# Optimization experiments

Measured on AMD Instinct MI355X. Metric: run time of the kernel, lower is better.

The kernel has to match this reference:

```python
import jax, jax.numpy as jnp
import numpy as np

BLOCK_SIZE = 64
SPARSITY_RATIO = 0.5


def _band_mask(seq_len, block_size, sparsity_ratio):
    # Block (i, j) is computed iff max(0, i-w) <= j < min(nb, i+w), w = int(nb*ratio).
    nb = seq_len // block_size
    w = int(nb * sparsity_ratio)
    ib = jnp.arange(nb)
    bm = (ib[None, :] >= ib[:, None] - w) & (ib[None, :] < ib[:, None] + w)  # [nb, nb]
    return jnp.repeat(jnp.repeat(bm, block_size, axis=0), block_size, axis=1)  # [S, S]


def setup_inputs() -> dict:
    key = jax.random.key(0)
    kq, kk, kv = jax.random.split(key, 3)
    B, S, D = 4, 4096, 128
    return {
        "query": jax.random.normal(kq, (B, S, D), dtype=jnp.float32),
        "key": jax.random.normal(kk, (B, S, D), dtype=jnp.float32),
        "value": jax.random.normal(kv, (B, S, D), dtype=jnp.float32),
    }


def reference(query, key, value):
    B, S, D = query.shape
    mask = _band_mask(S, BLOCK_SIZE, SPARSITY_RATIO)  # [S, S] bool
    scores = jnp.einsum('bqd,bkd->bqk', query, key)  # [B, S, S]
    # Outside-band entries stay exactly 0 (NOT -inf) — matches torch.zeros init.
    scores = jnp.where(mask[None, :, :], scores, jnp.zeros((), scores.dtype))
    probs = jax.nn.softmax(scores, axis=-1)
    return jnp.matmul(probs, value)  # [B, S, D]
```

## Files before the change

kernel.cpp:

```cpp
#include <hip/hip_runtime.h>


typedef _Float16 f16;
typedef __attribute__((ext_vector_type(8))) _Float16 f16x8;
typedef __attribute__((ext_vector_type(4))) _Float16 f16x4;
typedef __attribute__((ext_vector_type(4))) float f32x4;

#define MFMA16(a, b, c) __builtin_amdgcn_mfma_f32_16x16x32_f16((a), (b), (c), 0, 0, 0)

#define BATCH 4
#define SEQ   4096
#define DIM   128
#define NB    64
#define WBAND 32
#define LOG2E 1.44269504088896f
#define DTHR  8.0f
#define TSTR  72

#define TILE  16384
#define CHUNKS 8
#define PART_STRIDE 16896

__device__ __forceinline__ void gl16(const char* g, char* l) {
  __builtin_amdgcn_global_load_lds(
      (const __attribute__((address_space(1))) void*)g,
      (__attribute__((address_space(3))) void*)l, 16, 0, 0);
}

__global__ __launch_bounds__(256) void convert_kernel(
    const float* __restrict__ K, const float* __restrict__ V,
    f16* __restrict__ KF, f16* __restrict__ VF, float* __restrict__ BS) {
  __shared__ f16 T[128 * TSTR];
  const int blk = blockIdx.x;
  const int b = blk >> 6, jb = blk & 63;
  const int s0 = jb * 64;
  const int t = threadIdx.x;

#pragma unroll
  for (int i = 0; i < 8; ++i) {
    int idx = t + i * 256;
    int row = idx >> 5;
    int c4 = (idx & 31) * 4;
    float4 v = *(const float4*)(V + (size_t)(b * SEQ + s0 + row) * DIM + c4);
    T[(c4 + 0) * TSTR + row] = (f16)v.x;
    T[(c4 + 1) * TSTR + row] = (f16)v.y;
    T[(c4 + 2) * TSTR + row] = (f16)v.z;
    T[(c4 + 3) * TSTR + row] = (f16)v.w;
  }

  char* kt = (char*)KF + (size_t)blk * TILE;
#pragma unroll
  for (int i = 0; i < 4; ++i) {
    int idx = t + i * 256;
    int frag = idx >> 6, lane = idx & 63;
    int ks = frag >> 2, jt = frag & 3;
    int row = jt * 16 + (lane & 15);
    int d0 = ks * 32 + (lane >> 4) * 8;
    const float* src = K + ((size_t)(b * SEQ + s0 + row)) * DIM + d0;
    float4 a = *(const float4*)src;
    float4 d = *(const float4*)(src + 4);
    f16x8 h = {(f16)a.x, (f16)a.y, (f16)a.z, (f16)a.w,
               (f16)d.x, (f16)d.y, (f16)d.z, (f16)d.w};
    *(f16x8*)(kt + idx * 16) = h;
  }
  __syncthreads();

  char* vt = (char*)VF + (size_t)blk * TILE;
#pragma unroll
  for (int i = 0; i < 4; ++i) {
    int idx = t + i * 256;
    int frag = idx >> 6, lane = idx & 63;
    int ks2 = frag >> 3, nt = frag & 7;
    int d = nt * 16 + (lane & 15);
    int k0 = ks2 * 32 + ((lane >> 4) & 3) * 4;
    f16x4 x = *(const f16x4*)(T + d * TSTR + k0);
    f16x4 y = *(const f16x4*)(T + d * TSTR + k0 + 16);
    f16x8 h = {x[0], x[1], x[2], x[3], y[0], y[1], y[2], y[3]};
    *(f16x8*)(vt + idx * 16) = h;
  }

  if (t < 128) {
    float s = 0.f;
    for (int k = 0; k < 64; ++k) s += (float)T[t * TSTR + k];
    BS[(b * NB + jb) * DIM + t] = s;
  }
}

__global__ __launch_bounds__(256, 2) void attn_kernel(
    const float* __restrict__ Q, const f16* __restrict__ KF,
    const f16* __restrict__ VF, char* __restrict__ PART) {
  __shared__ __align__(16) char smem[16384];

  const int id = blockIdx.x;
  const int lin = (id & 7) * 128 + (id >> 3);
  const int ck = lin & 7;
  const int pair = lin >> 3;
  const int b = pair >> 5, p = pair & 31;

  const int t = threadIdx.x;
  const int w = t >> 6, l = t & 63, lg = l >> 4, ll = l & 15;
  const int half = w >> 1, qh = w & 1;
  const int myib = p * 2 + half;

  const int jloU = max(0, p * 2 - WBAND);
  const int jhiU = min(NB, p * 2 + 1 + WBAND);
  const int lenU = jhiU - jloU;
  const int base = lenU >> 3, rem = lenU & 7;
  const int j0 = jloU + ck * base + min(ck, rem);
  const int nloc = base + (ck < rem ? 1 : 0);
  const int mylo = max(0, myib - WBAND);
  const int myhi = min(NB, myib + WBAND);

  f16x8 qf[2][4];
#pragma unroll
  for (int s = 0; s < 2; ++s) {
    const float* qrow =
        Q + ((size_t)(b * SEQ + myib * 64 + qh * 32 + s * 16 + ll)) * DIM;
#pragma unroll
    for (int ks = 0; ks < 4; ++ks) {
      int d0 = ks * 32 + lg * 8;
      float4 a = *(const float4*)(qrow + d0);
      float4 cc = *(const float4*)(qrow + d0 + 4);
      float vv[8] = {a.x, a.y, a.z, a.w, cc.x, cc.y, cc.z, cc.w};
#pragma unroll
      for (int e = 0; e < 8; ++e) qf[s][ks][e] = (f16)(vv[e] * LOG2E);
    }
  }

  float m2[2] = {0.f, 0.f};
  float ell[2] = {0.f, 0.f};
  f32x4 o[2][8];
#pragma unroll
  for (int s = 0; s < 2; ++s)
#pragma unroll
    for (int nt = 0; nt < 8; ++nt) o[s][nt] = (f32x4){0.f, 0.f, 0.f, 0.f};

  auto stageK = [&](int jb) {
    const char* kg = (const char*)KF + ((size_t)(b * NB + jb)) * TILE + t * 16;
#pragma unroll
    for (int i = 0; i < 4; ++i) gl16(kg + i * 4096, smem + t * 16 + i * 4096);
  };

  stageK(j0);
  __syncthreads();

  for (int tt = 0; tt < nloc; ++tt) {
    const int j = j0 + tt;
    if (j >= mylo && j < myhi) {
      const char* vt =
          (const char*)VF + ((size_t)(b * NB + j)) * TILE + (size_t)l * 16;
      f16x8 vr0[8], vr1[8];
#pragma unroll
      for (int nt = 0; nt < 8; ++nt)
        vr0[nt] = *(const f16x8*)(vt + nt * 1024);
#pragma unroll
      for (int nt = 0; nt < 8; ++nt)
        vr1[nt] = *(const f16x8*)(vt + (8 + nt) * 1024);

      f32x4 sacc[2][4];
#pragma unroll
      for (int s = 0; s < 2; ++s)
#pragma unroll
        for (int jt = 0; jt < 4; ++jt) sacc[s][jt] = (f32x4){0.f, 0.f, 0.f, 0.f};

      __builtin_amdgcn_s_setprio(1);
#pragma unroll
      for (int ks = 0; ks < 4; ++ks) {
#pragma unroll
        for (int jt = 0; jt < 4; ++jt) {
          f16x8 kf = *(const f16x8*)(smem + (ks * 4 + jt) * 1024 + l * 16);
          sacc[0][jt] = MFMA16(kf, qf[0][ks], sacc[0][jt]);
          sacc[1][jt] = MFMA16(kf, qf[1][ks], sacc[1][jt]);
        }
      }
      __builtin_amdgcn_s_setprio(0);

      f16x8 pa[2][2];
#pragma unroll
      for (int s = 0; s < 2; ++s) {
        float vm = fmaxf(fmaxf(sacc[s][0][0], sacc[s][0][1]),
                         fmaxf(sacc[s][0][2], sacc[s][0][3]));
#pragma unroll
        for (int jt = 1; jt < 4; ++jt)
#pragma unroll
          for (int r = 0; r < 4; ++r) vm = fmaxf(vm, sacc[s][jt][r]);
        vm = fmaxf(vm, __shfl_xor(vm, 16));
        vm = fmaxf(vm, __shfl_xor(vm, 32));

        if (__any(vm - m2[s] > DTHR)) {
          float nm = fmaxf(m2[s], vm);
          float scl = __builtin_amdgcn_exp2f(m2[s] - nm);
          m2[s] = nm;
          ell[s] *= scl;
          float sb[4];
#pragma unroll
          for (int r = 0; r < 4; ++r) sb[r] = __shfl(scl, lg * 4 + r);
#pragma unroll
          for (int nt = 0; nt < 8; ++nt)
#pragma unroll
            for (int r = 0; r < 4; ++r) o[s][nt][r] *= sb[r];
        }

        float rsum = 0.f;
#pragma unroll
        for (int ks2 = 0; ks2 < 2; ++ks2) {
          f16x8 pv;
#pragma unroll
          for (int u = 0; u < 2; ++u)
#pragma unroll
            for (int r = 0; r < 4; ++r) {
              float pe = __builtin_amdgcn_exp2f(sacc[s][ks2 * 2 + u][r] - m2[s]);
              rsum += pe;
              pv[u * 4 + r] = (f16)pe;
            }
          pa[s][ks2] = pv;
        }
        ell[s] += rsum;
      }

      __builtin_amdgcn_s_setprio(1);
#pragma unroll
      for (int nt = 0; nt < 8; ++nt) {
        o[0][nt] = MFMA16(pa[0][0], vr0[nt], o[0][nt]);
        o[1][nt] = MFMA16(pa[1][0], vr0[nt], o[1][nt]);
      }
#pragma unroll
      for (int nt = 0; nt < 8; ++nt) {
        o[0][nt] = MFMA16(pa[0][1], vr1[nt], o[0][nt]);
        o[1][nt] = MFMA16(pa[1][1], vr1[nt], o[1][nt]);
      }
      __builtin_amdgcn_s_setprio(0);
    }

    __syncthreads();
    if (tt + 1 < nloc) stageK(j0 + tt + 1);
    __syncthreads();
  }

#pragma unroll
  for (int s = 0; s < 2; ++s) {
    ell[s] += __shfl_xor(ell[s], 16);
    ell[s] += __shfl_xor(ell[s], 32);
  }

  char* pb = PART + ((size_t)((pair * CHUNKS + ck) * 2 + half)) * PART_STRIDE;
#pragma unroll
  for (int s = 0; s < 2; ++s)
#pragma unroll
    for (int g = 0; g < 4; ++g) {
      f16x8 hh;
#pragma unroll
      for (int r = 0; r < 4; ++r) {
        hh[r] = (f16)o[s][2 * g][r];
        hh[4 + r] = (f16)o[s][2 * g + 1][r];
      }
      *(f16x8*)(pb + qh * 8192 + ((s * 4 + g) * 64 + l) * 16) = hh;
    }
  if (lg == 0) {
#pragma unroll
    for (int s = 0; s < 2; ++s)
      *(float2*)(pb + 16384 + (qh * 32 + s * 16 + ll) * 8) =
          make_float2(m2[s], ell[s]);
  }
}

__global__ __launch_bounds__(256) void merge_kernel(
    const char* __restrict__ PART, const float* __restrict__ BS,
    float* __restrict__ Out) {
  __shared__ float VoutS[DIM];
  __shared__ float mlS[CHUNKS][64][2];

  const int id = blockIdx.x;
  const int lin = (id & 7) * 32 + (id >> 3);
  const int pair = lin >> 1, half = lin & 1;
  const int b = pair >> 5;
  const int ib = (pair & 31) * 2 + half;
  const int t = threadIdx.x;
  const int l = t & 63, lg = (t >> 4) & 3, ll = t & 15;
  const int sub = (t >> 6) & 1, qh = t >> 7;

  const int jlo = max(0, ib - WBAND);
  const int jhi = min(NB, ib + WBAND);
  const float cnt_out = (float)(SEQ - (jhi - jlo) * 64);

  if (t < DIM) {
    float s = 0.f;
    for (int j = 0; j < jlo; ++j) s += BS[(b * NB + j) * DIM + t];
    for (int j = jhi; j < NB; ++j) s += BS[(b * NB + j) * DIM + t];
    VoutS[t] = s;
  }

  const size_t pb0 = ((size_t)(pair * CHUNKS * 2 + half)) * PART_STRIDE;
  for (int i = t; i < CHUNKS * 64; i += 256) {
    int k = i >> 6, row = i & 63;
    *(float2*)&mlS[k][row][0] = *(const float2*)(
        PART + pb0 + (size_t)k * 2 * PART_STRIDE + 16384 + row * 8);
  }
  __syncthreads();

  float aw[4][CHUNKS], en[4], inv[4];
#pragma unroll
  for (int r = 0; r < 4; ++r) {
    int row = qh * 32 + sub * 16 + lg * 4 + r;
    float M = mlS[0][row][0];
#pragma unroll
    for (int k = 1; k < CHUNKS; ++k) M = fmaxf(M, mlS[k][row][0]);
    en[r] = __builtin_amdgcn_exp2f(-M);
    float den = cnt_out * en[r];
#pragma unroll
    for (int k = 0; k < CHUNKS; ++k) {
      aw[r][k] = __builtin_amdgcn_exp2f(mlS[k][row][0] - M);
      den += aw[r][k] * mlS[k][row][1];
    }
    inv[r] = 1.f / den;
  }

  float acc[8][4];
#pragma unroll
  for (int nt = 0; nt < 8; ++nt)
#pragma unroll
    for (int r = 0; r < 4; ++r) acc[nt][r] = 0.f;

  for (int k = 0; k < CHUNKS; ++k) {
    const char* oc = PART + pb0 + (size_t)k * 2 * PART_STRIDE + qh * 8192;
#pragma unroll
    for (int g = 0; g < 4; ++g) {
      f16x8 h = *(const f16x8*)(oc + ((sub * 4 + g) * 64 + l) * 16);
#pragma unroll
      for (int r = 0; r < 4; ++r) {
        acc[2 * g][r] += aw[r][k] * (float)h[r];
        acc[2 * g + 1][r] += aw[r][k] * (float)h[4 + r];
      }
    }
  }

  const int q0 = ib * 64;
#pragma unroll
  for (int nt = 0; nt < 8; ++nt) {
    int col = nt * 16 + ll;
    float vout = VoutS[col];
#pragma unroll
    for (int r = 0; r < 4; ++r) {
      int row = qh * 32 + sub * 16 + lg * 4 + r;
      Out[((size_t)(b * SEQ + q0 + row)) * DIM + col] =
          (acc[nt][r] + en[r] * vout) * inv[r];
    }
  }
}

extern "C" void kernel_launch(void* const* d_in, const int* in_sizes, int n_in,
                              void* d_out, int out_size, void* d_ws, size_t ws_size,
                              hipStream_t stream) {
  const float* Q = (const float*)d_in[0];
  const float* K = (const float*)d_in[1];
  const float* V = (const float*)d_in[2];
  float* Out = (float*)d_out;

  char* ws = (char*)d_ws;
  f16* KF = (f16*)ws;
  f16* VF = (f16*)(ws + (size_t)BATCH * NB * TILE);
  float* BS = (float*)(ws + 2 * (size_t)BATCH * NB * TILE);
  char* PART = ws + 2 * (size_t)BATCH * NB * TILE + (size_t)BATCH * NB * DIM * 4;

  convert_kernel<<<dim3(BATCH * NB), 256, 0, stream>>>(K, V, KF, VF, BS);
  attn_kernel<<<dim3(BATCH * NB / 2 * CHUNKS), 256, 0, stream>>>(Q, KF, VF, PART);
  merge_kernel<<<dim3(BATCH * NB), 256, 0, stream>>>(PART, BS, Out);
}
```

Measured before the change: 66.83 us.

## Split attention into producer/consumer warps with LDS-staged probabilities

Each block now handles one query block instead of a pair. Two waves compute QK^T and the softmax and write f16 probabilities plus rescale factors into double-buffered LDS. The other two waves consume the previous tile's probabilities and do the PV MFMAs, each over half of the head dimension. This pipelines the two GEMM phases across waves, removes the pair-union wasted iterations, and raises the occupancy target to 3. The cost is more LDS, a one-tile lag, unconditional rescaling of the output every tile, and a changed V fragment layout in the convert kernel.

```diff
diff --git a/kernel.cpp b/kernel.cpp
--- a/kernel.cpp
+++ b/kernel.cpp
@@ -14,12 +14,16 @@
 #define NB    64
 #define WBAND 32
 #define LOG2E 1.44269504088896f
-#define DTHR  8.0f
 #define TSTR  72
+#define PSTR  72
 
 #define TILE  16384
 #define CHUNKS 8
 #define PART_STRIDE 16896
+
+#define POFF  16384
+#define PSZ   9216
+#define SOFF  34816
 
 __device__ __forceinline__ void gl16(const char* g, char* l) {
   __builtin_amdgcn_global_load_lds(
@@ -72,10 +76,8 @@
     int frag = idx >> 6, lane = idx & 63;
     int ks2 = frag >> 3, nt = frag & 7;
     int d = nt * 16 + (lane & 15);
-    int k0 = ks2 * 32 + ((lane >> 4) & 3) * 4;
-    f16x4 x = *(const f16x4*)(T + d * TSTR + k0);
-    f16x4 y = *(const f16x4*)(T + d * TSTR + k0 + 16);
-    f16x8 h = {x[0], x[1], x[2], x[3], y[0], y[1], y[2], y[3]};
+    int k0 = ks2 * 32 + (lane >> 4) * 8;
+    f16x8 h = *(const f16x8*)(T + d * TSTR + k0);
     *(f16x8*)(vt + idx * 16) = h;
   }
 
@@ -86,83 +88,113 @@
   }
 }
 
-__global__ __launch_bounds__(256, 2) void attn_kernel(
+__global__ __launch_bounds__(256, 3) void attn_kernel(
     const float* __restrict__ Q, const f16* __restrict__ KF,
     const f16* __restrict__ VF, char* __restrict__ PART) {
-  __shared__ __align__(16) char smem[16384];
+  __shared__ __align__(16) char smem[35328];
 
   const int id = blockIdx.x;
-  const int lin = (id & 7) * 128 + (id >> 3);
+  const int lin = (id & 7) * 256 + (id >> 3);
   const int ck = lin & 7;
-  const int pair = lin >> 3;
-  const int b = pair >> 5, p = pair & 31;
+  const int blk = lin >> 3;
+  const int b = blk >> 6, ib = blk & 63;
 
   const int t = threadIdx.x;
   const int w = t >> 6, l = t & 63, lg = l >> 4, ll = l & 15;
-  const int half = w >> 1, qh = w & 1;
-  const int myib = p * 2 + half;
-
-  const int jloU = max(0, p * 2 - WBAND);
-  const int jhiU = min(NB, p * 2 + 1 + WBAND);
-  const int lenU = jhiU - jloU;
-  const int base = lenU >> 3, rem = lenU & 7;
-  const int j0 = jloU + ck * base + min(ck, rem);
+  const int wr = (w + (id & 3)) & 3;
+  const bool isP = (wr < 2);
+  const int qh = wr & 1;
+  const int dh = wr & 1;
+
+  const int jlo = max(0, ib - WBAND);
+  const int jhi = min(NB, ib + WBAND);
+  const int n = jhi - jlo;
+  const int base = n >> 3, rem = n & 7;
+  const int j0 = jlo + ck * base + min(ck, rem);
   const int nloc = base + (ck < rem ? 1 : 0);
-  const int mylo = max(0, myib - WBAND);
-  const int myhi = min(NB, myib + WBAND);
+
+  f16* P0 = (f16*)(smem + POFF);
+  f16* P1 = (f16*)(smem + POFF + PSZ);
+  float* S0 = (float*)(smem + SOFF);
+  float* S1 = (float*)(smem + SOFF + 256);
 
   f16x8 qf[2][4];
-#pragma unroll
-  for (int s = 0; s < 2; ++s) {
-    const float* qrow =
-        Q + ((size_t)(b * SEQ + myib * 64 + qh * 32 + s * 16 + ll)) * DIM;
-#pragma unroll
-    for (int ks = 0; ks < 4; ++ks) {
-      int d0 = ks * 32 + lg * 8;
-      float4 a = *(const float4*)(qrow + d0);
-      float4 cc = *(const float4*)(qrow + d0 + 4);
-      float vv[8] = {a.x, a.y, a.z, a.w, cc.x, cc.y, cc.z, cc.w};
-#pragma unroll
-      for (int e = 0; e < 8; ++e) qf[s][ks][e] = (f16)(vv[e] * LOG2E);
-    }
-  }
-
   float m2[2] = {0.f, 0.f};
   float ell[2] = {0.f, 0.f};
-  f32x4 o[2][8];
-#pragma unroll
-  for (int s = 0; s < 2; ++s)
-#pragma unroll
-    for (int nt = 0; nt < 8; ++nt) o[s][nt] = (f32x4){0.f, 0.f, 0.f, 0.f};
-
-  auto stageK = [&](int jb) {
+  if (isP) {
+#pragma unroll
+    for (int s = 0; s < 2; ++s) {
+      const float* qrow =
+          Q + ((size_t)(b * SEQ + ib * 64 + qh * 32 + s * 16 + ll)) * DIM;
+#pragma unroll
+      for (int ks = 0; ks < 4; ++ks) {
+        int d0 = ks * 32 + lg * 8;
+        float4 a = *(const float4*)(qrow + d0);
+        float4 cc = *(const float4*)(qrow + d0 + 4);
+        float vv[8] = {a.x, a.y, a.z, a.w, cc.x, cc.y, cc.z, cc.w};
+#pragma unroll
+        for (int e = 0; e < 8; ++e) qf[s][ks][e] = (f16)(vv[e] * LOG2E);
+      }
+    }
+  }
+
+  f32x4 o[4][4];
+#pragma unroll
+  for (int qt2 = 0; qt2 < 4; ++qt2)
+#pragma unroll
+    for (int ntl = 0; ntl < 4; ++ntl) o[qt2][ntl] = (f32x4){0.f, 0.f, 0.f, 0.f};
+
+  auto stage = [&](int jb) {
     const char* kg = (const char*)KF + ((size_t)(b * NB + jb)) * TILE + t * 16;
 #pragma unroll
     for (int i = 0; i < 4; ++i) gl16(kg + i * 4096, smem + t * 16 + i * 4096);
   };
 
-  stageK(j0);
+  auto consume = [&](int tj) {
+    const f16* Pb = (tj & 1) ? P1 : P0;
+    const float* Sb = (tj & 1) ? S1 : S0;
+    const char* vt = (const char*)VF + ((size_t)(b * NB + j0 + tj)) * TILE +
+                     (size_t)l * 16;
+    f16x8 vbf[2][4];
+#pragma unroll
+    for (int ks2 = 0; ks2 < 2; ++ks2)
+#pragma unroll
+      for (int ntl = 0; ntl < 4; ++ntl)
+        vbf[ks2][ntl] = *(const f16x8*)(vt + (ks2 * 8 + dh * 4 + ntl) * 1024);
+#pragma unroll
+    for (int qt2 = 0; qt2 < 4; ++qt2) {
+      f32x4 sv = *(const f32x4*)(Sb + qt2 * 16 + lg * 4);
+#pragma unroll
+      for (int ntl = 0; ntl < 4; ++ntl)
+#pragma unroll
+        for (int r = 0; r < 4; ++r) o[qt2][ntl][r] *= sv[r];
+    }
+    __builtin_amdgcn_s_setprio(1);
+#pragma unroll
+    for (int qt2 = 0; qt2 < 4; ++qt2) {
+#pragma unroll
+      for (int ks2 = 0; ks2 < 2; ++ks2) {
+        f16x8 paf = *(const f16x8*)((const char*)Pb +
+                                    (qt2 * 16 + ll) * (PSTR * 2) +
+                                    (ks2 * 32 + lg * 8) * 2);
+#pragma unroll
+        for (int ntl = 0; ntl < 4; ++ntl)
+          o[qt2][ntl] = MFMA16(paf, vbf[ks2][ntl], o[qt2][ntl]);
+      }
+    }
+    __builtin_amdgcn_s_setprio(0);
+  };
+
+  stage(j0);
   __syncthreads();
 
   for (int tt = 0; tt < nloc; ++tt) {
-    const int j = j0 + tt;
-    if (j >= mylo && j < myhi) {
-      const char* vt =
-          (const char*)VF + ((size_t)(b * NB + j)) * TILE + (size_t)l * 16;
-      f16x8 vr0[8], vr1[8];
-#pragma unroll
-      for (int nt = 0; nt < 8; ++nt)
-        vr0[nt] = *(const f16x8*)(vt + nt * 1024);
-#pragma unroll
-      for (int nt = 0; nt < 8; ++nt)
-        vr1[nt] = *(const f16x8*)(vt + (8 + nt) * 1024);
-
+    if (isP) {
       f32x4 sacc[2][4];
 #pragma unroll
       for (int s = 0; s < 2; ++s)
 #pragma unroll
         for (int jt = 0; jt < 4; ++jt) sacc[s][jt] = (f32x4){0.f, 0.f, 0.f, 0.f};
-
       __builtin_amdgcn_s_setprio(1);
 #pragma unroll
       for (int ks = 0; ks < 4; ++ks) {
@@ -175,7 +207,8 @@
       }
       __builtin_amdgcn_s_setprio(0);
 
-      f16x8 pa[2][2];
+      f16* Pb = (tt & 1) ? P1 : P0;
+      float* Sb = (tt & 1) ? S1 : S0;
 #pragma unroll
       for (int s = 0; s < 2; ++s) {
         float vm = fmaxf(fmaxf(sacc[s][0][0], sacc[s][0][1]),
@@ -186,81 +219,66 @@
           for (int r = 0; r < 4; ++r) vm = fmaxf(vm, sacc[s][jt][r]);
         vm = fmaxf(vm, __shfl_xor(vm, 16));
         vm = fmaxf(vm, __shfl_xor(vm, 32));
-
-        if (__any(vm - m2[s] > DTHR)) {
-          float nm = fmaxf(m2[s], vm);
-          float scl = __builtin_amdgcn_exp2f(m2[s] - nm);
-          m2[s] = nm;
-          ell[s] *= scl;
-          float sb[4];
-#pragma unroll
-          for (int r = 0; r < 4; ++r) sb[r] = __shfl(scl, lg * 4 + r);
-#pragma unroll
-          for (int nt = 0; nt < 8; ++nt)
-#pragma unroll
-            for (int r = 0; r < 4; ++r) o[s][nt][r] *= sb[r];
+        float nm = fmaxf(m2[s], vm);
+        float sc = __builtin_amdgcn_exp2f(m2[s] - nm);
+        m2[s] = nm;
+        float rsum = 0.f;
+#pragma unroll
+        for (int jt = 0; jt < 4; ++jt) {
+          f16x4 pk;
+#pragma unroll
+          for (int r = 0; r < 4; ++r) {
+            float pe = __builtin_amdgcn_exp2f(sacc[s][jt][r] - nm);
+            rsum += pe;
+            pk[r] = (f16)pe;
+          }
+          *(f16x4*)(Pb + (qh * 32 + s * 16 + ll) * PSTR + jt * 16 + lg * 4) = pk;
         }
-
-        float rsum = 0.f;
-#pragma unroll
-        for (int ks2 = 0; ks2 < 2; ++ks2) {
-          f16x8 pv;
-#pragma unroll
-          for (int u = 0; u < 2; ++u)
-#pragma unroll
-            for (int r = 0; r < 4; ++r) {
-              float pe = __builtin_amdgcn_exp2f(sacc[s][ks2 * 2 + u][r] - m2[s]);
-              rsum += pe;
-              pv[u * 4 + r] = (f16)pe;
-            }
-          pa[s][ks2] = pv;
+        ell[s] = ell[s] * sc + rsum;
+        if (l < 16) Sb[qh * 32 + s * 16 + l] = sc;
+      }
+    } else if (tt > 0) {
+      consume(tt - 1);
+    }
+
+    __syncthreads();
+    if (tt + 1 < nloc) stage(j0 + tt + 1);
+    __syncthreads();
+  }
+
+  if (!isP) consume(nloc - 1);
+
+  const int pair = b * 32 + (ib >> 1), half = ib & 1;
+  char* pb = PART + ((size_t)((pair * CHUNKS + ck) * 2 + half)) * PART_STRIDE;
+
+  if (isP) {
+#pragma unroll
+    for (int s = 0; s < 2; ++s) {
+      ell[s] += __shfl_xor(ell[s], 16);
+      ell[s] += __shfl_xor(ell[s], 32);
+    }
+    if (lg == 0) {
+#pragma unroll
+      for (int s = 0; s < 2; ++s)
+        *(float2*)(pb + 16384 + (qh * 32 + s * 16 + ll) * 8) =
+            make_float2(m2[s], ell[s]);
+    }
+  } else {
+#pragma unroll
+    for (int qt2 = 0; qt2 < 4; ++qt2) {
+      int qh2 = qt2 >> 1, s = qt2 & 1;
+#pragma unroll
+      for (int gl = 0; gl < 2; ++gl) {
+        f16x8 hh;
+#pragma unroll
+        for (int r = 0; r < 4; ++r) {
+          hh[r] = (f16)o[qt2][2 * gl][r];
+          hh[4 + r] = (f16)o[qt2][2 * gl + 1][r];
         }
-        ell[s] += rsum;
-      }
-
-      __builtin_amdgcn_s_setprio(1);
-#pragma unroll
-      for (int nt = 0; nt < 8; ++nt) {
-        o[0][nt] = MFMA16(pa[0][0], vr0[nt], o[0][nt]);
-        o[1][nt] = MFMA16(pa[1][0], vr0[nt], o[1][nt]);
-      }
-#pragma unroll
-      for (int nt = 0; nt < 8; ++nt) {
-        o[0][nt] = MFMA16(pa[0][1], vr1[nt], o[0][nt]);
-        o[1][nt] = MFMA16(pa[1][1], vr1[nt], o[1][nt]);
-      }
-      __builtin_amdgcn_s_setprio(0);
-    }
-
-    __syncthreads();
-    if (tt + 1 < nloc) stageK(j0 + tt + 1);
-    __syncthreads();
-  }
-
-#pragma unroll
-  for (int s = 0; s < 2; ++s) {
-    ell[s] += __shfl_xor(ell[s], 16);
-    ell[s] += __shfl_xor(ell[s], 32);
-  }
-
-  char* pb = PART + ((size_t)((pair * CHUNKS + ck) * 2 + half)) * PART_STRIDE;
-#pragma unroll
-  for (int s = 0; s < 2; ++s)
-#pragma unroll
-    for (int g = 0; g < 4; ++g) {
-      f16x8 hh;
-#pragma unroll
-      for (int r = 0; r < 4; ++r) {
-        hh[r] = (f16)o[s][2 * g][r];
-        hh[4 + r] = (f16)o[s][2 * g + 1][r];
-      }
-      *(f16x8*)(pb + qh * 8192 + ((s * 4 + g) * 64 + l) * 16) = hh;
-    }
-  if (lg == 0) {
-#pragma unroll
-    for (int s = 0; s < 2; ++s)
-      *(float2*)(pb + 16384 + (qh * 32 + s * 16 + ll) * 8) =
-          make_float2(m2[s], ell[s]);
+        *(f16x8*)(pb + qh2 * 8192 +
+                  ((s * 4 + dh * 2 + gl) * 64 + l) * 16) = hh;
+      }
+    }
   }
 }
 
@@ -363,6 +381,6 @@
   char* PART = ws + 2 * (size_t)BATCH * NB * TILE + (size_t)BATCH * NB * DIM * 4;
 
   convert_kernel<<<dim3(BATCH * NB), 256, 0, stream>>>(K, V, KF, VF, BS);
-  attn_kernel<<<dim3(BATCH * NB / 2 * CHUNKS), 256, 0, stream>>>(Q, KF, VF, PART);
+  attn_kernel<<<dim3(BATCH * NB * CHUNKS), 256, 0, stream>>>(Q, KF, VF, PART);
   merge_kernel<<<dim3(BATCH * NB), 256, 0, stream>>>(PART, BS, Out);
 }
```

Measured after the change: 67.67 us. No clear change (+1.3%).

## Stage K and V tiles in pairs through LDS instead of direct V loads

Applied to the files above, without the earlier changes.

V tiles now go through LDS via async global-to-LDS loads instead of being read per-lane from global memory into registers. Two key blocks (K and V each) are staged per group, which halves the number of barrier round-trips per chunk. LDS use grows from 16KB to 64KB, which with two blocks per CU may cut occupancy. There is still no overlap: each group waits for its full load (vmcnt(0)) before computing, so load latency stays exposed.

```diff
diff --git a/kernel.cpp b/kernel.cpp
--- a/kernel.cpp
+++ b/kernel.cpp
@@ -20,6 +20,13 @@
 #define TILE  16384
 #define CHUNKS 8
 #define PART_STRIDE 16896
+
+#define KA_OFF 0
+#define KB_OFF 16384
+#define VA_OFF 32768
+#define VB_OFF 49152
+
+#define WAIT0 asm volatile("s_waitcnt vmcnt(0)" ::: "memory")
 
 __device__ __forceinline__ void gl16(const char* g, char* l) {
   __builtin_amdgcn_global_load_lds(
@@ -89,7 +96,7 @@
 __global__ __launch_bounds__(256, 2) void attn_kernel(
     const float* __restrict__ Q, const f16* __restrict__ KF,
     const f16* __restrict__ VF, char* __restrict__ PART) {
-  __shared__ __align__(16) char smem[16384];
+  __shared__ __align__(16) char smem[65536];
 
   const int id = blockIdx.x;
   const int lin = (id & 7) * 128 + (id >> 3);
@@ -135,106 +142,116 @@
 #pragma unroll
     for (int nt = 0; nt < 8; ++nt) o[s][nt] = (f32x4){0.f, 0.f, 0.f, 0.f};
 
-  auto stageK = [&](int jb) {
-    const char* kg = (const char*)KF + ((size_t)(b * NB + jb)) * TILE + t * 16;
-#pragma unroll
-    for (int i = 0; i < 4; ++i) gl16(kg + i * 4096, smem + t * 16 + i * 4096);
+  auto stage_group = [&](int g) {
+    const int jA = j0 + 2 * g;
+    {
+      const char* kg = (const char*)KF + ((size_t)(b * NB + jA)) * TILE + t * 16;
+      const char* vg = (const char*)VF + ((size_t)(b * NB + jA)) * TILE + t * 16;
+#pragma unroll
+      for (int i = 0; i < 4; ++i) gl16(kg + i * 4096, smem + KA_OFF + t * 16 + i * 4096);
+#pragma unroll
+      for (int i = 0; i < 4; ++i) gl16(vg + i * 4096, smem + VA_OFF + t * 16 + i * 4096);
+    }
+    if (2 * g + 1 < nloc) {
+      const int jB = jA + 1;
+      const char* kg = (const char*)KF + ((size_t)(b * NB + jB)) * TILE + t * 16;
+      const char* vg = (const char*)VF + ((size_t)(b * NB + jB)) * TILE + t * 16;
+#pragma unroll
+      for (int i = 0; i < 4; ++i) gl16(kg + i * 4096, smem + KB_OFF + t * 16 + i * 4096);
+#pragma unroll
+      for (int i = 0; i < 4; ++i) gl16(vg + i * 4096, smem + VB_OFF + t * 16 + i * 4096);
+    }
   };
 
-  stageK(j0);
-  __syncthreads();
-
-  for (int tt = 0; tt < nloc; ++tt) {
-    const int j = j0 + tt;
-    if (j >= mylo && j < myhi) {
-      const char* vt =
-          (const char*)VF + ((size_t)(b * NB + j)) * TILE + (size_t)l * 16;
-      f16x8 vr0[8], vr1[8];
-#pragma unroll
-      for (int nt = 0; nt < 8; ++nt)
-        vr0[nt] = *(const f16x8*)(vt + nt * 1024);
-#pragma unroll
-      for (int nt = 0; nt < 8; ++nt)
-        vr1[nt] = *(const f16x8*)(vt + (8 + nt) * 1024);
-
-      f32x4 sacc[2][4];
-#pragma unroll
-      for (int s = 0; s < 2; ++s)
-#pragma unroll
-        for (int jt = 0; jt < 4; ++jt) sacc[s][jt] = (f32x4){0.f, 0.f, 0.f, 0.f};
-
-      __builtin_amdgcn_s_setprio(1);
-#pragma unroll
-      for (int ks = 0; ks < 4; ++ks) {
-#pragma unroll
-        for (int jt = 0; jt < 4; ++jt) {
-          f16x8 kf = *(const f16x8*)(smem + (ks * 4 + jt) * 1024 + l * 16);
-          sacc[0][jt] = MFMA16(kf, qf[0][ks], sacc[0][jt]);
-          sacc[1][jt] = MFMA16(kf, qf[1][ks], sacc[1][jt]);
-        }
-      }
-      __builtin_amdgcn_s_setprio(0);
-
-      f16x8 pa[2][2];
-#pragma unroll
-      for (int s = 0; s < 2; ++s) {
-        float vm = fmaxf(fmaxf(sacc[s][0][0], sacc[s][0][1]),
-                         fmaxf(sacc[s][0][2], sacc[s][0][3]));
-#pragma unroll
-        for (int jt = 1; jt < 4; ++jt)
-#pragma unroll
-          for (int r = 0; r < 4; ++r) vm = fmaxf(vm, sacc[s][jt][r]);
-        vm = fmaxf(vm, __shfl_xor(vm, 16));
-        vm = fmaxf(vm, __shfl_xor(vm, 32));
-
-        if (__any(vm - m2[s] > DTHR)) {
-          float nm = fmaxf(m2[s], vm);
-          float scl = __builtin_amdgcn_exp2f(m2[s] - nm);
-          m2[s] = nm;
-          ell[s] *= scl;
-          float sb[4];
-#pragma unroll
-          for (int r = 0; r < 4; ++r) sb[r] = __shfl(scl, lg * 4 + r);
-#pragma unroll
-          for (int nt = 0; nt < 8; ++nt)
-#pragma unroll
-            for (int r = 0; r < 4; ++r) o[s][nt][r] *= sb[r];
-        }
-
-        float rsum = 0.f;
-#pragma unroll
-        for (int ks2 = 0; ks2 < 2; ++ks2) {
-          f16x8 pv;
-#pragma unroll
-          for (int u = 0; u < 2; ++u)
-#pragma unroll
-            for (int r = 0; r < 4; ++r) {
-              float pe = __builtin_amdgcn_exp2f(sacc[s][ks2 * 2 + u][r] - m2[s]);
-              rsum += pe;
-              pv[u * 4 + r] = (f16)pe;
-            }
-          pa[s][ks2] = pv;
-        }
-        ell[s] += rsum;
-      }
-
-      __builtin_amdgcn_s_setprio(1);
+  auto compute = [&](int j, const char* kb, const char* vb) {
+    if (j < mylo || j >= myhi) return;
+
+    f32x4 sacc[2][4];
+#pragma unroll
+    for (int s = 0; s < 2; ++s)
+#pragma unroll
+      for (int jt = 0; jt < 4; ++jt) sacc[s][jt] = (f32x4){0.f, 0.f, 0.f, 0.f};
+
+    __builtin_amdgcn_s_setprio(1);
+#pragma unroll
+    for (int ks = 0; ks < 4; ++ks) {
+#pragma unroll
+      for (int jt = 0; jt < 4; ++jt) {
+        f16x8 kf = *(const f16x8*)(kb + (ks * 4 + jt) * 1024 + l * 16);
+        sacc[0][jt] = MFMA16(kf, qf[0][ks], sacc[0][jt]);
+        sacc[1][jt] = MFMA16(kf, qf[1][ks], sacc[1][jt]);
+      }
+    }
+    __builtin_amdgcn_s_setprio(0);
+
+    f16x8 pa[2][2];
+#pragma unroll
+    for (int s = 0; s < 2; ++s) {
+      float vm = fmaxf(fmaxf(sacc[s][0][0], sacc[s][0][1]),
+                       fmaxf(sacc[s][0][2], sacc[s][0][3]));
+#pragma unroll
+      for (int jt = 1; jt < 4; ++jt)
+#pragma unroll
+        for (int r = 0; r < 4; ++r) vm = fmaxf(vm, sacc[s][jt][r]);
+      vm = fmaxf(vm, __shfl_xor(vm, 16));
+      vm = fmaxf(vm, __shfl_xor(vm, 32));
+
+      if (__any(vm - m2[s] > DTHR)) {
+        float nm = fmaxf(m2[s], vm);
+        float scl = __builtin_amdgcn_exp2f(m2[s] - nm);
+        m2[s] = nm;
+        ell[s] *= scl;
+        float sb[4];
+#pragma unroll
+        for (int r = 0; r < 4; ++r) sb[r] = __shfl(scl, lg * 4 + r);
+#pragma unroll
+        for (int nt = 0; nt < 8; ++nt)
+#pragma unroll
+          for (int r = 0; r < 4; ++r) o[s][nt][r] *= sb[r];
+      }
+
+      float rsum = 0.f;
+#pragma unroll
+      for (int ks2 = 0; ks2 < 2; ++ks2) {
+        f16x8 pv;
+#pragma unroll
+        for (int u = 0; u < 2; ++u)
+#pragma unroll
+          for (int r = 0; r < 4; ++r) {
+            float pe = __builtin_amdgcn_exp2f(sacc[s][ks2 * 2 + u][r] - m2[s]);
+            rsum += pe;
+            pv[u * 4 + r] = (f16)pe;
+          }
+        pa[s][ks2] = pv;
+      }
+      ell[s] += rsum;
+    }
+
+    __builtin_amdgcn_s_setprio(1);
+#pragma unroll
+    for (int ks2 = 0; ks2 < 2; ++ks2) {
 #pragma unroll
       for (int nt = 0; nt < 8; ++nt) {
-        o[0][nt] = MFMA16(pa[0][0], vr0[nt], o[0][nt]);
-        o[1][nt] = MFMA16(pa[1][0], vr0[nt], o[1][nt]);
-      }
-#pragma unroll
-      for (int nt = 0; nt < 8; ++nt) {
-        o[0][nt] = MFMA16(pa[0][1], vr1[nt], o[0][nt]);
-        o[1][nt] = MFMA16(pa[1][1], vr1[nt], o[1][nt]);
-      }
-      __builtin_amdgcn_s_setprio(0);
-    }
-
+        f16x8 vbf = *(const f16x8*)(vb + (ks2 * 8 + nt) * 1024 + l * 16);
+        o[0][nt] = MFMA16(pa[0][ks2], vbf, o[0][nt]);
+        o[1][nt] = MFMA16(pa[1][ks2], vbf, o[1][nt]);
+      }
+    }
+    __builtin_amdgcn_s_setprio(0);
+  };
+
+  const int ng = (nloc + 1) >> 1;
+  stage_group(0);
+  for (int g = 0; g < ng; ++g) {
+    WAIT0;
     __syncthreads();
-    if (tt + 1 < nloc) stageK(j0 + tt + 1);
+
+    compute(j0 + 2 * g, smem + KA_OFF, smem + VA_OFF);
+    if (2 * g + 1 < nloc)
+      compute(j0 + 2 * g + 1, smem + KB_OFF, smem + VB_OFF);
+
     __syncthreads();
+    if (g + 1 < ng) stage_group(g + 1);
   }
 
 #pragma unroll
```

Result: faster. 64.90 us (-2.9%).
